# Optimization experiments

Measured on AMD Instinct MI355X. Metric: run time of the kernel, lower is better.

Reference implementation:

```python
import jax, jax.numpy as jnp
import numpy as np

B, T, D, C = 8, 4096, 768, 2048

def setup_inputs() -> dict:
    key = jax.random.key(0)
    k1, k2 = jax.random.split(key)
    embed = jax.random.normal(k1, (B, T, D), dtype=jnp.float32)
    cluster_centers = jax.random.normal(k2, (C, D), dtype=jnp.float32)
    return {"embed": embed, "cluster_centers": cluster_centers}

def reference(embed, cluster_centers):
    x_sq = jnp.sum(embed * embed, axis=-1, keepdims=True)          # (b, t, 1)
    c_sq = jnp.sum(cluster_centers * cluster_centers, axis=-1)     # (c,)
    cross = jnp.einsum('btd,cd->btc', embed, cluster_centers)      # (b, t, c)
    sq_dists = x_sq + c_sq[None, None, :] - 2.0 * cross
    dists = jnp.sqrt(jnp.maximum(sq_dists, 0.0))
    # dists argmax of -cdist == argmin of cdist
    clusters = jnp.argmin(dists, axis=-1)                          # (b, t) int
    return clusters
```

## Files before the change

### kernel.cpp

```cpp
#include <hip/hip_runtime.h>

typedef __fp16 f16x2 __attribute__((ext_vector_type(2)));
typedef __fp16 f16x8 __attribute__((ext_vector_type(8)));
typedef float f32x4 __attribute__((ext_vector_type(4)));

constexpr int MM = 32768;
constexpr int NN = 2048;
constexpr int KK = 768;
constexpr int BM = 128;
constexpr int BN = 128;
constexpr int BK = 32;
constexpr int RSTR = KK * 2 / 16;

constexpr size_t WS_AH   = 0;
constexpr size_t WS_AL   = WS_AH + (size_t)MM * KK * 2;
constexpr size_t WS_BH   = WS_AL + (size_t)MM * KK * 2;
constexpr size_t WS_BL   = WS_BH + (size_t)NN * KK * 2;
constexpr size_t WS_CSQ  = WS_BL + (size_t)NN * KK * 2;
constexpr size_t WS_SLOT = WS_CSQ + (size_t)NN * 4;
constexpr size_t WS_NEED = WS_SLOT + (size_t)MM * 16 * 8;

__device__ __forceinline__ unsigned bc(f16x2 h) {
    return __builtin_bit_cast(unsigned, h);
}


__global__ __launch_bounds__(256)
void preconvert_kernel(const float* __restrict__ A, const float* __restrict__ Bc,
                       unsigned short* __restrict__ AhG, unsigned short* __restrict__ AlG,
                       unsigned short* __restrict__ BhG, unsigned short* __restrict__ BlG,
                       float* __restrict__ csq) {
    const int bid = blockIdx.x;
    const bool isB = bid >= (MM / 32);
    const int rowbase = (isB ? bid - MM / 32 : bid) * 32;
    const int tid = threadIdx.x;
    const int row = tid >> 3, kc = tid & 7;
    const size_t base = (size_t)(rowbase + row) * KK + kc * 8;
    const float* src = (isB ? Bc : A) + base;
    unsigned short* dh = (isB ? BhG : AhG) + base;
    unsigned short* dl = (isB ? BlG : AlG) + base;

    float s = 0.f;
#pragma unroll
    for (int t = 0; t < 12; ++t) {
        float4 v0 = *(const float4*)(src + t * 64);
        float4 v1 = *(const float4*)(src + t * 64 + 4);
        if (isB) {
            s = fmaf(v0.x, v0.x, s); s = fmaf(v0.y, v0.y, s);
            s = fmaf(v0.z, v0.z, s); s = fmaf(v0.w, v0.w, s);
            s = fmaf(v1.x, v1.x, s); s = fmaf(v1.y, v1.y, s);
            s = fmaf(v1.z, v1.z, s); s = fmaf(v1.w, v1.w, s);
        }
        f16x2 h0 = __builtin_amdgcn_cvt_pkrtz(v0.x, v0.y);
        f16x2 h1 = __builtin_amdgcn_cvt_pkrtz(v0.z, v0.w);
        f16x2 h2 = __builtin_amdgcn_cvt_pkrtz(v1.x, v1.y);
        f16x2 h3 = __builtin_amdgcn_cvt_pkrtz(v1.z, v1.w);
        f16x2 l0 = __builtin_amdgcn_cvt_pkrtz(v0.x-(float)h0[0], v0.y-(float)h0[1]);
        f16x2 l1 = __builtin_amdgcn_cvt_pkrtz(v0.z-(float)h1[0], v0.w-(float)h1[1]);
        f16x2 l2 = __builtin_amdgcn_cvt_pkrtz(v1.x-(float)h2[0], v1.y-(float)h2[1]);
        f16x2 l3 = __builtin_amdgcn_cvt_pkrtz(v1.z-(float)h3[0], v1.w-(float)h3[1]);
        uint4 hv = {bc(h0), bc(h1), bc(h2), bc(h3)};
        uint4 lv = {bc(l0), bc(l1), bc(l2), bc(l3)};
        *(uint4*)(dh + t * 64) = hv;
        *(uint4*)(dl + t * 64) = lv;
    }
    if (isB) {
        s += __shfl_xor(s, 1, 64);
        s += __shfl_xor(s, 2, 64);
        s += __shfl_xor(s, 4, 64);
        if (kc == 0) csq[rowbase + row] = s;
    }
}

__global__ __launch_bounds__(256, 2)
void gemm_f16_kernel(const unsigned short* __restrict__ AhG, const unsigned short* __restrict__ AlG,
                     const unsigned short* __restrict__ BhG, const unsigned short* __restrict__ BlG,
                     const float* __restrict__ csq, uint2* __restrict__ slots) {
    __shared__ unsigned lds[4 * 128 * 20];
    constexpr int AH = 0, AL = 2560, BH = 5120, BL = 7680;

    const int tid  = threadIdx.x;
    const int lane = tid & 63;
    const int ln15 = lane & 15;
    const int quad = lane >> 4;
    const int wave = tid >> 6;
    const int wm = wave >> 1, wn = wave & 1;
    const int tbase = blockIdx.x * BM;
    const int cb    = blockIdx.y * BN;

    const int r0 = tid >> 2, ku = tid & 3;
    const uint4* gAh = (const uint4*)AhG;
    const uint4* gAl = (const uint4*)AlG;
    const uint4* gBh = (const uint4*)BhG;
    const uint4* gBl = (const uint4*)BlG;
    const size_t arow0 = (size_t)(tbase + r0) * RSTR + ku;
    const size_t arow1 = (size_t)(tbase + r0 + 64) * RSTR + ku;
    const size_t brow0 = (size_t)(cb + r0) * RSTR + ku;
    const size_t brow1 = (size_t)(cb + r0 + 64) * RSTR + ku;
    const int sw0 = r0 * 20 + ku * 4;
    const int sw1 = sw0 + 64 * 20;

    f32x4 acc[4][4];
#pragma unroll
    for (int i = 0; i < 4; ++i)
#pragma unroll
        for (int j = 0; j < 4; ++j) { f32x4 z = {0.f,0.f,0.f,0.f}; acc[i][j] = z; }

    uint4 pAh0 = gAh[arow0], pAh1 = gAh[arow1];
    uint4 pAl0 = gAl[arow0], pAl1 = gAl[arow1];
    uint4 pBh0 = gBh[brow0], pBh1 = gBh[brow1];
    uint4 pBl0 = gBl[brow0], pBl1 = gBl[brow1];

    int aw[4], bw[4];
#pragma unroll
    for (int i = 0; i < 4; ++i) {
        aw[i] = AH + (wm * 64 + i * 16 + ln15) * 20 + quad * 4;
        bw[i] = BH + (wn * 64 + i * 16 + ln15) * 20 + quad * 4;
    }

    for (int kt = 0; kt < KK / BK; ++kt) {
        __syncthreads();
        *(uint4*)&lds[AH + sw0] = pAh0; *(uint4*)&lds[AH + sw1] = pAh1;
        *(uint4*)&lds[AL + sw0] = pAl0; *(uint4*)&lds[AL + sw1] = pAl1;
        *(uint4*)&lds[BH + sw0] = pBh0; *(uint4*)&lds[BH + sw1] = pBh1;
        *(uint4*)&lds[BL + sw0] = pBl0; *(uint4*)&lds[BL + sw1] = pBl1;
        __syncthreads();

        if (kt + 1 < KK / BK) {
            const size_t ko = (size_t)(kt + 1) * 4;
            pAh0 = gAh[arow0 + ko]; pAh1 = gAh[arow1 + ko];
            pAl0 = gAl[arow0 + ko]; pAl1 = gAl[arow1 + ko];
            pBh0 = gBh[brow0 + ko]; pBh1 = gBh[brow1 + ko];
            pBl0 = gBl[brow0 + ko]; pBl1 = gBl[brow1 + ko];
        }

        f16x8 a_h[4], a_l[4], b_h[4], b_l[4];
#pragma unroll
        for (int i = 0; i < 4; ++i) {
            a_h[i] = *(const f16x8*)&lds[aw[i]];
            a_l[i] = *(const f16x8*)&lds[aw[i] + (AL - AH)];
            b_h[i] = *(const f16x8*)&lds[bw[i]];
            b_l[i] = *(const f16x8*)&lds[bw[i] + (BL - BH)];
        }
#pragma unroll
        for (int i = 0; i < 4; ++i)
#pragma unroll
            for (int j = 0; j < 4; ++j) {
                acc[i][j] = __builtin_amdgcn_mfma_f32_16x16x32_f16(a_h[i], b_h[j], acc[i][j], 0, 0, 0);
                acc[i][j] = __builtin_amdgcn_mfma_f32_16x16x32_f16(a_h[i], b_l[j], acc[i][j], 0, 0, 0);
                acc[i][j] = __builtin_amdgcn_mfma_f32_16x16x32_f16(a_l[i], b_h[j], acc[i][j], 0, 0, 0);
            }
    }

    float csq4[4];
#pragma unroll
    for (int j = 0; j < 4; ++j) csq4[j] = csq[cb + wn * 64 + j * 16 + ln15];

    float bval[16]; int bidx[16];
#pragma unroll
    for (int i = 0; i < 4; ++i)
#pragma unroll
        for (int r = 0; r < 4; ++r) {
            const int rid = i * 4 + r;
            float bv_ = csq4[0] - 2.0f * acc[i][0][r];
            int   bi_ = cb + wn * 64 + ln15;
#pragma unroll
            for (int j = 1; j < 4; ++j) {
                const float s = csq4[j] - 2.0f * acc[i][j][r];
                const int   c = cb + wn * 64 + j * 16 + ln15;
                if (s < bv_) { bv_ = s; bi_ = c; }
            }
            bval[rid] = bv_; bidx[rid] = bi_;
        }
#pragma unroll
    for (int off = 1; off < 16; off <<= 1) {
#pragma unroll
        for (int rid = 0; rid < 16; ++rid) {
            const float ov = __shfl_xor(bval[rid], off, 64);
            const int   oi = __shfl_xor(bidx[rid], off, 64);
            if (ov < bval[rid] || (ov == bval[rid] && oi < bidx[rid])) {
                bval[rid] = ov; bidx[rid] = oi;
            }
        }
    }

    __syncthreads();
    float* vtab = (float*)&lds[0];
    int*   itab = (int*)&lds[256];
    if (ln15 == 0) {
#pragma unroll
        for (int i = 0; i < 4; ++i)
#pragma unroll
            for (int r = 0; r < 4; ++r) {
                const int row = wm * 64 + i * 16 + quad * 4 + r;
                vtab[row * 2 + wn] = bval[i * 4 + r];
                itab[row * 2 + wn] = bidx[i * 4 + r];
            }
    }
    __syncthreads();
    if (tid < 128) {
        float v0 = vtab[tid * 2]; int i0 = itab[tid * 2];
        const float v1 = vtab[tid * 2 + 1]; const int i1 = itab[tid * 2 + 1];
        if (v1 < v0 || (v1 == v0 && i1 < i0)) { v0 = v1; i0 = i1; }
        uint2 e; e.x = __float_as_uint(v0); e.y = (unsigned)i0;
        slots[(size_t)(tbase + tid) * 16 + blockIdx.y] = e;
    }
}

__global__ __launch_bounds__(256)
void slot_reduce_kernel(const uint2* __restrict__ slots, int* __restrict__ out) {
    const int t = blockIdx.x * 256 + threadIdx.x;
    const uint2* s = slots + (size_t)t * 16;
    float bv = __uint_as_float(s[0].x); int bi = (int)s[0].y;
#pragma unroll
    for (int j = 1; j < 16; ++j) {
        const uint2 e = s[j];
        const float v = __uint_as_float(e.x);
        if (v < bv || (v == bv && (int)e.y < bi)) { bv = v; bi = (int)e.y; }
    }
    out[t] = bi;
}


__global__ __launch_bounds__(256)
void init_ws_kernel(unsigned long long* __restrict__ w) {
    w[blockIdx.x * 256 + threadIdx.x] = 0xFFFFFFFFFFFFFFFFull;
}

__global__ __launch_bounds__(64)
void csq_kernel(const float* __restrict__ cc, float* __restrict__ csq) {
    const int cl = blockIdx.x;
    const int lane = threadIdx.x;
    const float4* row = reinterpret_cast<const float4*>(cc + (size_t)cl * KK);
    float s = 0.f;
#pragma unroll
    for (int w = 0; w < KK / (4 * 64); ++w) {
        float4 v = row[w * 64 + lane];
        s = fmaf(v.x, v.x, s); s = fmaf(v.y, v.y, s);
        s = fmaf(v.z, v.z, s); s = fmaf(v.w, v.w, s);
    }
#pragma unroll
    for (int off = 32; off > 0; off >>= 1) s += __shfl_xor(s, off, 64);
    if (lane == 0) csq[cl] = s;
}

__global__ __launch_bounds__(256, 2)
void argmin_mfma_kernel(const float* __restrict__ A, const float* __restrict__ Bc,
                        const float* __restrict__ csq,
                        unsigned long long* __restrict__ ws64) {
    __shared__ unsigned lds[4 * 128 * 20];
    constexpr int AH = 0, AL = 2560, BH = 5120;

    const int tid  = threadIdx.x;
    const int lane = tid & 63;
    const int ln15 = lane & 15;
    const int quad = lane >> 4;
    const int wave = tid >> 6;
    const int wm = wave >> 1, wn = wave & 1;
    const int tbase = blockIdx.x * BM;
    const int cb    = blockIdx.y * BN;

    const int sr  = tid >> 1;
    const int skh = tid & 1;
    const float* gA = A  + (size_t)(tbase + sr) * KK + skh * 16;
    const float* gB = Bc + (size_t)(cb   + sr) * KK + skh * 16;
    const int wword = sr * 20 + skh * 8;

    f32x4 acc[4][4];
#pragma unroll
    for (int i = 0; i < 4; ++i)
#pragma unroll
        for (int j = 0; j < 4; ++j) { f32x4 z = {0.f,0.f,0.f,0.f}; acc[i][j] = z; }

    float4 av[4], bv[4];
#pragma unroll
    for (int p = 0; p < 4; ++p) {
        av[p] = *(const float4*)(gA + p * 4);
        bv[p] = *(const float4*)(gB + p * 4);
    }

    int aw[4], bw[4];
#pragma unroll
    for (int i = 0; i < 4; ++i) {
        aw[i] = AH + (wm * 64 + i * 16 + ln15) * 20 + quad * 4;
        bw[i] = BH + (wn * 64 + i * 16 + ln15) * 20 + quad * 4;
    }

    for (int k0 = 0; k0 < KK; k0 += BK) {
        __syncthreads();
#pragma unroll
        for (int h = 0; h < 2; ++h) {
            float4 v0 = av[2*h], v1 = av[2*h+1];
            f16x2 h00 = __builtin_amdgcn_cvt_pkrtz(v0.x, v0.y);
            f16x2 h01 = __builtin_amdgcn_cvt_pkrtz(v0.z, v0.w);
            f16x2 h10 = __builtin_amdgcn_cvt_pkrtz(v1.x, v1.y);
            f16x2 h11 = __builtin_amdgcn_cvt_pkrtz(v1.z, v1.w);
            f16x2 l00 = __builtin_amdgcn_cvt_pkrtz(v0.x-(float)h00[0], v0.y-(float)h00[1]);
            f16x2 l01 = __builtin_amdgcn_cvt_pkrtz(v0.z-(float)h01[0], v0.w-(float)h01[1]);
            f16x2 l10 = __builtin_amdgcn_cvt_pkrtz(v1.x-(float)h10[0], v1.y-(float)h10[1]);
            f16x2 l11 = __builtin_amdgcn_cvt_pkrtz(v1.z-(float)h11[0], v1.w-(float)h11[1]);
            uint4 hv = {bc(h00), bc(h01), bc(h10), bc(h11)};
            uint4 lv = {bc(l00), bc(l01), bc(l10), bc(l11)};
            *(uint4*)&lds[AH + wword + 4*h] = hv;
            *(uint4*)&lds[AL + wword + 4*h] = lv;

            float4 w0 = bv[2*h], w1 = bv[2*h+1];
            f16x2 g00 = __builtin_amdgcn_cvt_pkrtz(w0.x, w0.y);
            f16x2 g01 = __builtin_amdgcn_cvt_pkrtz(w0.z, w0.w);
            f16x2 g10 = __builtin_amdgcn_cvt_pkrtz(w1.x, w1.y);
            f16x2 g11 = __builtin_amdgcn_cvt_pkrtz(w1.z, w1.w);
            f16x2 m00 = __builtin_amdgcn_cvt_pkrtz(w0.x-(float)g00[0], w0.y-(float)g00[1]);
            f16x2 m01 = __builtin_amdgcn_cvt_pkrtz(w0.z-(float)g01[0], w0.w-(float)g01[1]);
            f16x2 m10 = __builtin_amdgcn_cvt_pkrtz(w1.x-(float)g10[0], w1.y-(float)g10[1]);
            f16x2 m11 = __builtin_amdgcn_cvt_pkrtz(w1.z-(float)g11[0], w1.w-(float)g11[1]);
            uint4 gv = {bc(g00), bc(g01), bc(g10), bc(g11)};
            uint4 mv = {bc(m00), bc(m01), bc(m10), bc(m11)};
            *(uint4*)&lds[BH + wword + 4*h]        = gv;
            *(uint4*)&lds[BH + 2560 + wword + 4*h] = mv;
        }
        __syncthreads();

        const int kn = k0 + BK;
        if (kn < KK) {
#pragma unroll
            for (int p = 0; p < 4; ++p) {
                av[p] = *(const float4*)(gA + kn + p * 4);
                bv[p] = *(const float4*)(gB + kn + p * 4);
            }
        }

        f16x8 a_h[4], a_l[4], b_h[4], b_l[4];
#pragma unroll
        for (int i = 0; i < 4; ++i) {
            a_h[i] = *(const f16x8*)&lds[aw[i]];
            a_l[i] = *(const f16x8*)&lds[aw[i] + 2560];
            b_h[i] = *(const f16x8*)&lds[bw[i]];
            b_l[i] = *(const f16x8*)&lds[bw[i] + 2560];
        }
#pragma unroll
        for (int i = 0; i < 4; ++i)
#pragma unroll
            for (int j = 0; j < 4; ++j) {
                acc[i][j] = __builtin_amdgcn_mfma_f32_16x16x32_f16(a_h[i], b_h[j], acc[i][j], 0, 0, 0);
                acc[i][j] = __builtin_amdgcn_mfma_f32_16x16x32_f16(a_h[i], b_l[j], acc[i][j], 0, 0, 0);
                acc[i][j] = __builtin_amdgcn_mfma_f32_16x16x32_f16(a_l[i], b_h[j], acc[i][j], 0, 0, 0);
            }
    }

    float csq4[4];
#pragma unroll
    for (int j = 0; j < 4; ++j) csq4[j] = csq[cb + wn * 64 + j * 16 + ln15];

    float bval[16]; int bidx[16];
#pragma unroll
    for (int i = 0; i < 4; ++i)
#pragma unroll
        for (int r = 0; r < 4; ++r) {
            const int rid = i * 4 + r;
            float bv_ = csq4[0] - 2.0f * acc[i][0][r];
            int   bi_ = cb + wn * 64 + ln15;
#pragma unroll
            for (int j = 1; j < 4; ++j) {
                const float s = csq4[j] - 2.0f * acc[i][j][r];
                const int   c = cb + wn * 64 + j * 16 + ln15;
                if (s < bv_) { bv_ = s; bi_ = c; }
            }
            bval[rid] = bv_; bidx[rid] = bi_;
        }
#pragma unroll
    for (int off = 1; off < 16; off <<= 1) {
#pragma unroll
        for (int rid = 0; rid < 16; ++rid) {
            const float ov = __shfl_xor(bval[rid], off, 64);
            const int   oi = __shfl_xor(bidx[rid], off, 64);
            if (ov < bval[rid] || (ov == bval[rid] && oi < bidx[rid])) {
                bval[rid] = ov; bidx[rid] = oi;
            }
        }
    }

    __syncthreads();
    float* vtab = (float*)&lds[0];
    int*   itab = (int*)&lds[256];
    if (ln15 == 0) {
#pragma unroll
        for (int i = 0; i < 4; ++i)
#pragma unroll
            for (int r = 0; r < 4; ++r) {
                const int row = wm * 64 + i * 16 + quad * 4 + r;
                vtab[row * 2 + wn] = bval[i * 4 + r];
                itab[row * 2 + wn] = bidx[i * 4 + r];
            }
    }
    __syncthreads();
    if (tid < 128) {
        float v0 = vtab[tid * 2]; int i0 = itab[tid * 2];
        const float v1 = vtab[tid * 2 + 1]; const int i1 = itab[tid * 2 + 1];
        if (v1 < v0 || (v1 == v0 && i1 < i0)) { v0 = v1; i0 = i1; }
        const unsigned b   = __float_as_uint(v0);
        const unsigned key = (b & 0x80000000u) ? ~b : (b | 0x80000000u);
        const unsigned long long pk =
            ((unsigned long long)key << 32) | (unsigned long long)(unsigned)i0;
        atomicMin(&ws64[tbase + tid], pk);
    }
}

__global__ __launch_bounds__(256)
void unpack_kernel(const unsigned long long* __restrict__ w, int* __restrict__ out) {
    const int i = blockIdx.x * 256 + threadIdx.x;
    out[i] = (int)(unsigned)(w[i] & 0xFFFFFFFFull);
}

extern "C" void kernel_launch(void* const* d_in, const int* in_sizes, int n_in,
                              void* d_out, int out_size, void* d_ws, size_t ws_size,
                              hipStream_t stream) {
    const float* embed   = (const float*)d_in[0];
    const float* centers = (const float*)d_in[1];
    int* out = (int*)d_out;

    if (ws_size >= WS_NEED) {
        unsigned short* Ah = (unsigned short*)((char*)d_ws + WS_AH);
        unsigned short* Al = (unsigned short*)((char*)d_ws + WS_AL);
        unsigned short* Bh = (unsigned short*)((char*)d_ws + WS_BH);
        unsigned short* Bl = (unsigned short*)((char*)d_ws + WS_BL);
        float* csq   = (float*)((char*)d_ws + WS_CSQ);
        uint2* slots = (uint2*)((char*)d_ws + WS_SLOT);
        preconvert_kernel<<<MM / 32 + NN / 32, 256, 0, stream>>>(
            embed, centers, Ah, Al, Bh, Bl, csq);
        gemm_f16_kernel<<<dim3(MM / BM, NN / BN), 256, 0, stream>>>(
            Ah, Al, Bh, Bl, csq, slots);
        slot_reduce_kernel<<<MM / 256, 256, 0, stream>>>(slots, out);
    } else {
        unsigned long long* ws64 = (unsigned long long*)d_ws;
        float* csq = (float*)((char*)d_ws + (size_t)MM * 8);
        init_ws_kernel<<<MM / 256, 256, 0, stream>>>(ws64);
        csq_kernel<<<NN, 64, 0, stream>>>(centers, csq);
        argmin_mfma_kernel<<<dim3(MM / BM, NN / BN), 256, 0, stream>>>(
            embed, centers, csq, ws64);
        unpack_kernel<<<MM / 256, 256, 0, stream>>>(ws64, out);
    }
}
```

Before: 495.0 us.

## Pre-pack operands into MFMA fragment layout and load directly into registers

The preconvert step now writes the hi/lo fp16 split of embed and centers in a per-16-row, per-32-K fragment-major layout, so each lane's MFMA operand is one contiguous uint4. The GEMM then skips LDS and barriers entirely, loading fragments straight from global memory into registers with a two-stage double buffer. The grid is swapped so the cluster tile varies fastest, letting consecutive blocks share the same embed rows in cache. Center norms move to a separate csq kernel. Without LDS, each wave re-reads its A/B fragments from global/L2 with no cross-wave sharing, and register pressure rises from the double-buffered fragments.

```diff
diff --git a/kernel.cpp b/kernel.cpp
--- a/kernel.cpp
+++ b/kernel.cpp
@@ -9,16 +9,15 @@
 constexpr int KK = 768;
 constexpr int BM = 128;
 constexpr int BN = 128;
-constexpr int BK = 32;
-constexpr int RSTR = KK * 2 / 16;
-
-constexpr size_t WS_AH   = 0;
-constexpr size_t WS_AL   = WS_AH + (size_t)MM * KK * 2;
-constexpr size_t WS_BH   = WS_AL + (size_t)MM * KK * 2;
-constexpr size_t WS_BL   = WS_BH + (size_t)NN * KK * 2;
-constexpr size_t WS_CSQ  = WS_BL + (size_t)NN * KK * 2;
-constexpr size_t WS_SLOT = WS_CSQ + (size_t)NN * 4;
-constexpr size_t WS_NEED = WS_SLOT + (size_t)MM * 16 * 8;
+constexpr int NKT = KK / 32;
+constexpr int NA_UNITS = (MM / 16) * NKT;
+constexpr int NB_UNITS = (NN / 16) * NKT;
+
+constexpr size_t WS_APACK = 0;
+constexpr size_t WS_BPACK = WS_APACK + (size_t)MM * KK * 4;
+constexpr size_t WS_CSQ   = WS_BPACK + (size_t)NN * KK * 4;
+constexpr size_t WS_SLOT  = WS_CSQ + (size_t)NN * 4;
+constexpr size_t WS_NEED  = WS_SLOT + (size_t)MM * 16 * 8;
 
 __device__ __forceinline__ unsigned bc(f16x2 h) {
     return __builtin_bit_cast(unsigned, h);
@@ -26,58 +25,212 @@
 
 
 __global__ __launch_bounds__(256)
-void preconvert_kernel(const float* __restrict__ A, const float* __restrict__ Bc,
-                       unsigned short* __restrict__ AhG, unsigned short* __restrict__ AlG,
-                       unsigned short* __restrict__ BhG, unsigned short* __restrict__ BlG,
-                       float* __restrict__ csq) {
-    const int bid = blockIdx.x;
-    const bool isB = bid >= (MM / 32);
-    const int rowbase = (isB ? bid - MM / 32 : bid) * 32;
-    const int tid = threadIdx.x;
-    const int row = tid >> 3, kc = tid & 7;
-    const size_t base = (size_t)(rowbase + row) * KK + kc * 8;
-    const float* src = (isB ? Bc : A) + base;
-    unsigned short* dh = (isB ? BhG : AhG) + base;
-    unsigned short* dl = (isB ? BlG : AlG) + base;
-
+void fragpack_kernel(const float* __restrict__ A, const float* __restrict__ Bc,
+                     uint4* __restrict__ Ap, uint4* __restrict__ Bp) {
+    const int task = blockIdx.x * 4 + (threadIdx.x >> 6);
+    const int lane = threadIdx.x & 63;
+    const int ln15 = lane & 15;
+    const int quad = lane >> 4;
+
+    const bool isB = task >= NA_UNITS;
+    const int t = isB ? task - NA_UNITS : task;
+    const int tile = t / NKT, kt = t % NKT;
+    const float* src = (isB ? Bc : A) + (size_t)(tile * 16 + ln15) * KK + kt * 32 + quad * 8;
+    uint4* dst = (isB ? Bp : Ap) + (size_t)t * 128 + lane;
+
+    const float4 v0 = *(const float4*)(src);
+    const float4 v1 = *(const float4*)(src + 4);
+    f16x2 h0 = __builtin_amdgcn_cvt_pkrtz(v0.x, v0.y);
+    f16x2 h1 = __builtin_amdgcn_cvt_pkrtz(v0.z, v0.w);
+    f16x2 h2 = __builtin_amdgcn_cvt_pkrtz(v1.x, v1.y);
+    f16x2 h3 = __builtin_amdgcn_cvt_pkrtz(v1.z, v1.w);
+    f16x2 l0 = __builtin_amdgcn_cvt_pkrtz(v0.x-(float)h0[0], v0.y-(float)h0[1]);
+    f16x2 l1 = __builtin_amdgcn_cvt_pkrtz(v0.z-(float)h1[0], v0.w-(float)h1[1]);
+    f16x2 l2 = __builtin_amdgcn_cvt_pkrtz(v1.x-(float)h2[0], v1.y-(float)h2[1]);
+    f16x2 l3 = __builtin_amdgcn_cvt_pkrtz(v1.z-(float)h3[0], v1.w-(float)h3[1]);
+    uint4 hv = {bc(h0), bc(h1), bc(h2), bc(h3)};
+    uint4 lv = {bc(l0), bc(l1), bc(l2), bc(l3)};
+    dst[0]  = hv;
+    dst[64] = lv;
+}
+
+__global__ __launch_bounds__(64)
+void csq_kernel(const float* __restrict__ cc, float* __restrict__ csq) {
+    const int cl = blockIdx.x;
+    const int lane = threadIdx.x;
+    const float4* row = reinterpret_cast<const float4*>(cc + (size_t)cl * KK);
     float s = 0.f;
 #pragma unroll
-    for (int t = 0; t < 12; ++t) {
-        float4 v0 = *(const float4*)(src + t * 64);
-        float4 v1 = *(const float4*)(src + t * 64 + 4);
-        if (isB) {
-            s = fmaf(v0.x, v0.x, s); s = fmaf(v0.y, v0.y, s);
-            s = fmaf(v0.z, v0.z, s); s = fmaf(v0.w, v0.w, s);
-            s = fmaf(v1.x, v1.x, s); s = fmaf(v1.y, v1.y, s);
-            s = fmaf(v1.z, v1.z, s); s = fmaf(v1.w, v1.w, s);
-        }
-        f16x2 h0 = __builtin_amdgcn_cvt_pkrtz(v0.x, v0.y);
-        f16x2 h1 = __builtin_amdgcn_cvt_pkrtz(v0.z, v0.w);
-        f16x2 h2 = __builtin_amdgcn_cvt_pkrtz(v1.x, v1.y);
-        f16x2 h3 = __builtin_amdgcn_cvt_pkrtz(v1.z, v1.w);
-        f16x2 l0 = __builtin_amdgcn_cvt_pkrtz(v0.x-(float)h0[0], v0.y-(float)h0[1]);
-        f16x2 l1 = __builtin_amdgcn_cvt_pkrtz(v0.z-(float)h1[0], v0.w-(float)h1[1]);
-        f16x2 l2 = __builtin_amdgcn_cvt_pkrtz(v1.x-(float)h2[0], v1.y-(float)h2[1]);
-        f16x2 l3 = __builtin_amdgcn_cvt_pkrtz(v1.z-(float)h3[0], v1.w-(float)h3[1]);
-        uint4 hv = {bc(h0), bc(h1), bc(h2), bc(h3)};
-        uint4 lv = {bc(l0), bc(l1), bc(l2), bc(l3)};
-        *(uint4*)(dh + t * 64) = hv;
-        *(uint4*)(dl + t * 64) = lv;
-    }
-    if (isB) {
-        s += __shfl_xor(s, 1, 64);
-        s += __shfl_xor(s, 2, 64);
-        s += __shfl_xor(s, 4, 64);
-        if (kc == 0) csq[rowbase + row] = s;
-    }
-}
+    for (int w = 0; w < KK / (4 * 64); ++w) {
+        float4 v = row[w * 64 + lane];
+        s = fmaf(v.x, v.x, s); s = fmaf(v.y, v.y, s);
+        s = fmaf(v.z, v.z, s); s = fmaf(v.w, v.w, s);
+    }
+#pragma unroll
+    for (int off = 32; off > 0; off >>= 1) s += __shfl_xor(s, off, 64);
+    if (lane == 0) csq[cl] = s;
+}
+
+#define MF(a, b, c) __builtin_amdgcn_mfma_f32_16x16x32_f16( \
+    __builtin_bit_cast(f16x8, a), __builtin_bit_cast(f16x8, b), c, 0, 0, 0)
 
 __global__ __launch_bounds__(256, 2)
-void gemm_f16_kernel(const unsigned short* __restrict__ AhG, const unsigned short* __restrict__ AlG,
-                     const unsigned short* __restrict__ BhG, const unsigned short* __restrict__ BlG,
-                     const float* __restrict__ csq, uint2* __restrict__ slots) {
+void gemm_pack_kernel(const uint4* __restrict__ Ap, const uint4* __restrict__ Bp,
+                      const float* __restrict__ csq, uint2* __restrict__ slots) {
+    const int gx = blockIdx.x;
+    const int gy = blockIdx.y;
+    const int tid  = threadIdx.x;
+    const int lane = tid & 63;
+    const int ln15 = lane & 15;
+    const int quad = lane >> 4;
+    const int wave = tid >> 6;
+    const int wm = wave >> 1, wn = wave & 1;
+    const int tbase = gy * BM;
+    const int cb    = gx * BN;
+
+    const uint4* a_ptr[4];
+    const uint4* b_ptr[4];
+#pragma unroll
+    for (int i = 0; i < 4; ++i) {
+        a_ptr[i] = Ap + (size_t)(gy * 8 + wm * 4 + i) * NKT * 128 + lane;
+        b_ptr[i] = Bp + (size_t)(gx * 8 + wn * 4 + i) * NKT * 128 + lane;
+    }
+
+    f32x4 acc[4][4];
+#pragma unroll
+    for (int i = 0; i < 4; ++i)
+#pragma unroll
+        for (int j = 0; j < 4; ++j) { f32x4 z = {0.f,0.f,0.f,0.f}; acc[i][j] = z; }
+
+    uint4 Ah0[4], Al0[4], Bh0[4], Bl0[4];
+    uint4 Ah1[4], Al1[4], Bh1[4], Bl1[4];
+
+    auto load0 = [&](int kt) {
+        const int o = kt * 128;
+#pragma unroll
+        for (int i = 0; i < 4; ++i) {
+            Ah0[i] = a_ptr[i][o]; Al0[i] = a_ptr[i][o + 64];
+            Bh0[i] = b_ptr[i][o]; Bl0[i] = b_ptr[i][o + 64];
+        }
+    };
+    auto load1 = [&](int kt) {
+        const int o = kt * 128;
+#pragma unroll
+        for (int i = 0; i < 4; ++i) {
+            Ah1[i] = a_ptr[i][o]; Al1[i] = a_ptr[i][o + 64];
+            Bh1[i] = b_ptr[i][o]; Bl1[i] = b_ptr[i][o + 64];
+        }
+    };
+    auto comp0 = [&]() {
+#pragma unroll
+        for (int i = 0; i < 4; ++i)
+#pragma unroll
+            for (int j = 0; j < 4; ++j) {
+                acc[i][j] = MF(Ah0[i], Bh0[j], acc[i][j]);
+                acc[i][j] = MF(Ah0[i], Bl0[j], acc[i][j]);
+                acc[i][j] = MF(Al0[i], Bh0[j], acc[i][j]);
+            }
+    };
+    auto comp1 = [&]() {
+#pragma unroll
+        for (int i = 0; i < 4; ++i)
+#pragma unroll
+            for (int j = 0; j < 4; ++j) {
+                acc[i][j] = MF(Ah1[i], Bh1[j], acc[i][j]);
+                acc[i][j] = MF(Ah1[i], Bl1[j], acc[i][j]);
+                acc[i][j] = MF(Al1[i], Bh1[j], acc[i][j]);
+            }
+    };
+
+    load0(0);
+#pragma unroll 1
+    for (int kt = 0; kt < NKT; kt += 2) {
+        load1(kt + 1);
+        comp0();
+        if (kt + 2 < NKT) load0(kt + 2);
+        comp1();
+    }
+
+    float csq4[4];
+#pragma unroll
+    for (int j = 0; j < 4; ++j) csq4[j] = csq[cb + wn * 64 + j * 16 + ln15];
+
+    float bval[16]; int bidx[16];
+#pragma unroll
+    for (int i = 0; i < 4; ++i)
+#pragma unroll
+        for (int r = 0; r < 4; ++r) {
+            const int rid = i * 4 + r;
+            float bv_ = csq4[0] - 2.0f * acc[i][0][r];
+            int   bi_ = cb + wn * 64 + ln15;
+#pragma unroll
+            for (int j = 1; j < 4; ++j) {
+                const float s = csq4[j] - 2.0f * acc[i][j][r];
+                const int   c = cb + wn * 64 + j * 16 + ln15;
+                if (s < bv_) { bv_ = s; bi_ = c; }
+            }
+            bval[rid] = bv_; bidx[rid] = bi_;
+        }
+#pragma unroll
+    for (int off = 1; off < 16; off <<= 1) {
+#pragma unroll
+        for (int rid = 0; rid < 16; ++rid) {
+            const float ov = __shfl_xor(bval[rid], off, 64);
+            const int   oi = __shfl_xor(bidx[rid], off, 64);
+            if (ov < bval[rid] || (ov == bval[rid] && oi < bidx[rid])) {
+                bval[rid] = ov; bidx[rid] = oi;
+            }
+        }
+    }
+
+    __shared__ float vtab[256];
+    __shared__ int   itab[256];
+    if (ln15 == 0) {
+#pragma unroll
+        for (int i = 0; i < 4; ++i)
+#pragma unroll
+            for (int r = 0; r < 4; ++r) {
+                const int row = wm * 64 + i * 16 + quad * 4 + r;
+                vtab[row * 2 + wn] = bval[i * 4 + r];
+                itab[row * 2 + wn] = bidx[i * 4 + r];
+            }
+    }
+    __syncthreads();
+    if (tid < 128) {
+        float v0 = vtab[tid * 2]; int i0 = itab[tid * 2];
+        const float v1 = vtab[tid * 2 + 1]; const int i1 = itab[tid * 2 + 1];
+        if (v1 < v0 || (v1 == v0 && i1 < i0)) { v0 = v1; i0 = i1; }
+        uint2 e; e.x = __float_as_uint(v0); e.y = (unsigned)i0;
+        slots[(size_t)(tbase + tid) * 16 + gx] = e;
+    }
+}
+
+__global__ __launch_bounds__(256)
+void slot_reduce_kernel(const uint2* __restrict__ slots, int* __restrict__ out) {
+    const int t = blockIdx.x * 256 + threadIdx.x;
+    const uint2* s = slots + (size_t)t * 16;
+    float bv = __uint_as_float(s[0].x); int bi = (int)s[0].y;
+#pragma unroll
+    for (int j = 1; j < 16; ++j) {
+        const uint2 e = s[j];
+        const float v = __uint_as_float(e.x);
+        if (v < bv || (v == bv && (int)e.y < bi)) { bv = v; bi = (int)e.y; }
+    }
+    out[t] = bi;
+}
+
+
+__global__ __launch_bounds__(256)
+void init_ws_kernel(unsigned long long* __restrict__ w) {
+    w[blockIdx.x * 256 + threadIdx.x] = 0xFFFFFFFFFFFFFFFFull;
+}
+
+__global__ __launch_bounds__(256, 2)
+void argmin_mfma_kernel(const float* __restrict__ A, const float* __restrict__ Bc,
+                        const float* __restrict__ csq,
+                        unsigned long long* __restrict__ ws64) {
     __shared__ unsigned lds[4 * 128 * 20];
-    constexpr int AH = 0, AL = 2560, BH = 5120, BL = 7680;
+    constexpr int AH = 0, AL = 2560, BH = 5120;
 
     const int tid  = threadIdx.x;
     const int lane = tid & 63;
@@ -88,178 +241,6 @@
     const int tbase = blockIdx.x * BM;
     const int cb    = blockIdx.y * BN;
 
-    const int r0 = tid >> 2, ku = tid & 3;
-    const uint4* gAh = (const uint4*)AhG;
-    const uint4* gAl = (const uint4*)AlG;
-    const uint4* gBh = (const uint4*)BhG;
-    const uint4* gBl = (const uint4*)BlG;
-    const size_t arow0 = (size_t)(tbase + r0) * RSTR + ku;
-    const size_t arow1 = (size_t)(tbase + r0 + 64) * RSTR + ku;
-    const size_t brow0 = (size_t)(cb + r0) * RSTR + ku;
-    const size_t brow1 = (size_t)(cb + r0 + 64) * RSTR + ku;
-    const int sw0 = r0 * 20 + ku * 4;
-    const int sw1 = sw0 + 64 * 20;
-
-    f32x4 acc[4][4];
-#pragma unroll
-    for (int i = 0; i < 4; ++i)
-#pragma unroll
-        for (int j = 0; j < 4; ++j) { f32x4 z = {0.f,0.f,0.f,0.f}; acc[i][j] = z; }
-
-    uint4 pAh0 = gAh[arow0], pAh1 = gAh[arow1];
-    uint4 pAl0 = gAl[arow0], pAl1 = gAl[arow1];
-    uint4 pBh0 = gBh[brow0], pBh1 = gBh[brow1];
-    uint4 pBl0 = gBl[brow0], pBl1 = gBl[brow1];
-
-    int aw[4], bw[4];
-#pragma unroll
-    for (int i = 0; i < 4; ++i) {
-        aw[i] = AH + (wm * 64 + i * 16 + ln15) * 20 + quad * 4;
-        bw[i] = BH + (wn * 64 + i * 16 + ln15) * 20 + quad * 4;
-    }
-
-    for (int kt = 0; kt < KK / BK; ++kt) {
-        __syncthreads();
-        *(uint4*)&lds[AH + sw0] = pAh0; *(uint4*)&lds[AH + sw1] = pAh1;
-        *(uint4*)&lds[AL + sw0] = pAl0; *(uint4*)&lds[AL + sw1] = pAl1;
-        *(uint4*)&lds[BH + sw0] = pBh0; *(uint4*)&lds[BH + sw1] = pBh1;
-        *(uint4*)&lds[BL + sw0] = pBl0; *(uint4*)&lds[BL + sw1] = pBl1;
-        __syncthreads();
-
-        if (kt + 1 < KK / BK) {
-            const size_t ko = (size_t)(kt + 1) * 4;
-            pAh0 = gAh[arow0 + ko]; pAh1 = gAh[arow1 + ko];
-            pAl0 = gAl[arow0 + ko]; pAl1 = gAl[arow1 + ko];
-            pBh0 = gBh[brow0 + ko]; pBh1 = gBh[brow1 + ko];
-            pBl0 = gBl[brow0 + ko]; pBl1 = gBl[brow1 + ko];
-        }
-
-        f16x8 a_h[4], a_l[4], b_h[4], b_l[4];
-#pragma unroll
-        for (int i = 0; i < 4; ++i) {
-            a_h[i] = *(const f16x8*)&lds[aw[i]];
-            a_l[i] = *(const f16x8*)&lds[aw[i] + (AL - AH)];
-            b_h[i] = *(const f16x8*)&lds[bw[i]];
-            b_l[i] = *(const f16x8*)&lds[bw[i] + (BL - BH)];
-        }
-#pragma unroll
-        for (int i = 0; i < 4; ++i)
-#pragma unroll
-            for (int j = 0; j < 4; ++j) {
-                acc[i][j] = __builtin_amdgcn_mfma_f32_16x16x32_f16(a_h[i], b_h[j], acc[i][j], 0, 0, 0);
-                acc[i][j] = __builtin_amdgcn_mfma_f32_16x16x32_f16(a_h[i], b_l[j], acc[i][j], 0, 0, 0);
-                acc[i][j] = __builtin_amdgcn_mfma_f32_16x16x32_f16(a_l[i], b_h[j], acc[i][j], 0, 0, 0);
-            }
-    }
-
-    float csq4[4];
-#pragma unroll
-    for (int j = 0; j < 4; ++j) csq4[j] = csq[cb + wn * 64 + j * 16 + ln15];
-
-    float bval[16]; int bidx[16];
-#pragma unroll
-    for (int i = 0; i < 4; ++i)
-#pragma unroll
-        for (int r = 0; r < 4; ++r) {
-            const int rid = i * 4 + r;
-            float bv_ = csq4[0] - 2.0f * acc[i][0][r];
-            int   bi_ = cb + wn * 64 + ln15;
-#pragma unroll
-            for (int j = 1; j < 4; ++j) {
-                const float s = csq4[j] - 2.0f * acc[i][j][r];
-                const int   c = cb + wn * 64 + j * 16 + ln15;
-                if (s < bv_) { bv_ = s; bi_ = c; }
-            }
-            bval[rid] = bv_; bidx[rid] = bi_;
-        }
-#pragma unroll
-    for (int off = 1; off < 16; off <<= 1) {
-#pragma unroll
-        for (int rid = 0; rid < 16; ++rid) {
-            const float ov = __shfl_xor(bval[rid], off, 64);
-            const int   oi = __shfl_xor(bidx[rid], off, 64);
-            if (ov < bval[rid] || (ov == bval[rid] && oi < bidx[rid])) {
-                bval[rid] = ov; bidx[rid] = oi;
-            }
-        }
-    }
-
-    __syncthreads();
-    float* vtab = (float*)&lds[0];
-    int*   itab = (int*)&lds[256];
-    if (ln15 == 0) {
-#pragma unroll
-        for (int i = 0; i < 4; ++i)
-#pragma unroll
-            for (int r = 0; r < 4; ++r) {
-                const int row = wm * 64 + i * 16 + quad * 4 + r;
-                vtab[row * 2 + wn] = bval[i * 4 + r];
-                itab[row * 2 + wn] = bidx[i * 4 + r];
-            }
-    }
-    __syncthreads();
-    if (tid < 128) {
-        float v0 = vtab[tid * 2]; int i0 = itab[tid * 2];
-        const float v1 = vtab[tid * 2 + 1]; const int i1 = itab[tid * 2 + 1];
-        if (v1 < v0 || (v1 == v0 && i1 < i0)) { v0 = v1; i0 = i1; }
-        uint2 e; e.x = __float_as_uint(v0); e.y = (unsigned)i0;
-        slots[(size_t)(tbase + tid) * 16 + blockIdx.y] = e;
-    }
-}
-
-__global__ __launch_bounds__(256)
-void slot_reduce_kernel(const uint2* __restrict__ slots, int* __restrict__ out) {
-    const int t = blockIdx.x * 256 + threadIdx.x;
-    const uint2* s = slots + (size_t)t * 16;
-    float bv = __uint_as_float(s[0].x); int bi = (int)s[0].y;
-#pragma unroll
-    for (int j = 1; j < 16; ++j) {
-        const uint2 e = s[j];
-        const float v = __uint_as_float(e.x);
-        if (v < bv || (v == bv && (int)e.y < bi)) { bv = v; bi = (int)e.y; }
-    }
-    out[t] = bi;
-}
-
-
-__global__ __launch_bounds__(256)
-void init_ws_kernel(unsigned long long* __restrict__ w) {
-    w[blockIdx.x * 256 + threadIdx.x] = 0xFFFFFFFFFFFFFFFFull;
-}
-
-__global__ __launch_bounds__(64)
-void csq_kernel(const float* __restrict__ cc, float* __restrict__ csq) {
-    const int cl = blockIdx.x;
-    const int lane = threadIdx.x;
-    const float4* row = reinterpret_cast<const float4*>(cc + (size_t)cl * KK);
-    float s = 0.f;
-#pragma unroll
-    for (int w = 0; w < KK / (4 * 64); ++w) {
-        float4 v = row[w * 64 + lane];
-        s = fmaf(v.x, v.x, s); s = fmaf(v.y, v.y, s);
-        s = fmaf(v.z, v.z, s); s = fmaf(v.w, v.w, s);
-    }
-#pragma unroll
-    for (int off = 32; off > 0; off >>= 1) s += __shfl_xor(s, off, 64);
-    if (lane == 0) csq[cl] = s;
-}
-
-__global__ __launch_bounds__(256, 2)
-void argmin_mfma_kernel(const float* __restrict__ A, const float* __restrict__ Bc,
-                        const float* __restrict__ csq,
-                        unsigned long long* __restrict__ ws64) {
-    __shared__ unsigned lds[4 * 128 * 20];
-    constexpr int AH = 0, AL = 2560, BH = 5120;
-
-    const int tid  = threadIdx.x;
-    const int lane = tid & 63;
-    const int ln15 = lane & 15;
-    const int quad = lane >> 4;
-    const int wave = tid >> 6;
-    const int wm = wave >> 1, wn = wave & 1;
-    const int tbase = blockIdx.x * BM;
-    const int cb    = blockIdx.y * BN;
-
     const int sr  = tid >> 1;
     const int skh = tid & 1;
     const float* gA = A  + (size_t)(tbase + sr) * KK + skh * 16;
@@ -286,7 +267,7 @@
         bw[i] = BH + (wn * 64 + i * 16 + ln15) * 20 + quad * 4;
     }
 
-    for (int k0 = 0; k0 < KK; k0 += BK) {
+    for (int k0 = 0; k0 < KK; k0 += 32) {
         __syncthreads();
 #pragma unroll
         for (int h = 0; h < 2; ++h) {
@@ -320,7 +301,7 @@
         }
         __syncthreads();
 
-        const int kn = k0 + BK;
+        const int kn = k0 + 32;
         if (kn < KK) {
 #pragma unroll
             for (int p = 0; p < 4; ++p) {
@@ -419,16 +400,15 @@
     int* out = (int*)d_out;
 
     if (ws_size >= WS_NEED) {
-        unsigned short* Ah = (unsigned short*)((char*)d_ws + WS_AH);
-        unsigned short* Al = (unsigned short*)((char*)d_ws + WS_AL);
-        unsigned short* Bh = (unsigned short*)((char*)d_ws + WS_BH);
-        unsigned short* Bl = (unsigned short*)((char*)d_ws + WS_BL);
+        uint4* Ap = (uint4*)((char*)d_ws + WS_APACK);
+        uint4* Bp = (uint4*)((char*)d_ws + WS_BPACK);
         float* csq   = (float*)((char*)d_ws + WS_CSQ);
         uint2* slots = (uint2*)((char*)d_ws + WS_SLOT);
-        preconvert_kernel<<<MM / 32 + NN / 32, 256, 0, stream>>>(
-            embed, centers, Ah, Al, Bh, Bl, csq);
-        gemm_f16_kernel<<<dim3(MM / BM, NN / BN), 256, 0, stream>>>(
-            Ah, Al, Bh, Bl, csq, slots);
+        fragpack_kernel<<<(NA_UNITS + NB_UNITS) / 4, 256, 0, stream>>>(
+            embed, centers, Ap, Bp);
+        csq_kernel<<<NN, 64, 0, stream>>>(centers, csq);
+        gemm_pack_kernel<<<dim3(NN / BN, MM / BM), 256, 0, stream>>>(
+            Ap, Bp, csq, slots);
         slot_reduce_kernel<<<MM / 256, 256, 0, stream>>>(slots, out);
     } else {
         unsigned long long* ws64 = (unsigned long long*)d_ws;
```

New measurement: 452.7 us. 1.09x faster.
